# Kernel tuning notes

Measured on AMD Instinct MI355X. Metric: run time of the kernel, lower is better.

The kernel has to match this reference:

```python
import jax, jax.numpy as jnp
import numpy as np

D_EEG_MAX = 10.0
H_FMRI_MAX = 5.0
CLZ_MAX = 3.0
D_MAX = 1.0  # config.diffusion_coefficient_range[1]
N_LEVELS = 8  # discretization levels -> 64 pair-histogram bins


def setup_inputs() -> dict:
    key = jax.random.key(0)
    k1, k2 = jax.random.split(key)
    B, E = 8192, 4096
    psi_distribution = jax.random.uniform(k1, (B, E), dtype=jnp.float32)
    fractal_field = jax.random.normal(k2, (B, E), dtype=jnp.float32)
    fci_weights = jnp.array([0.4, 0.3, 0.3], dtype=jnp.float32)
    return {"psi_distribution": psi_distribution,
            "fractal_field": fractal_field,
            "fci_weights": fci_weights}


def _d_eeg(psi):
    # entropy of P(psi) per row, averaged; torch.std is unbiased (ddof=1)
    entropy = -jnp.sum(psi * jnp.log(psi + 1e-10), axis=-1).mean()
    spatial_variation = jnp.std(psi, axis=-1, ddof=1).mean()
    return jnp.minimum(entropy * spatial_variation * 3.0, D_EEG_MAX)


def _spatial_correlation(field):
    # Pearson corr between adjacent feature columns over the batch, vectorized
    c = field - field.mean(axis=0, keepdims=True)          # [B, E]
    var = jnp.sum(c * c, axis=0)                            # [E]
    cov = jnp.sum(c[:, :-1] * c[:, 1:], axis=0)             # [E-1]
    corr = cov / jnp.sqrt(var[:-1] * var[1:])               # [E-1]
    mask = ~jnp.isnan(corr)                                 # torch code skips NaNs
    n = jnp.sum(mask)
    mean_corr = jnp.where(n > 0,
                          jnp.sum(jnp.where(mask, corr, 0.0)) / jnp.maximum(n, 1),
                          0.0)
    return jnp.abs(mean_corr)


def _h_fmri(field):
    field_magnitude = jnp.linalg.norm(field, axis=-1).mean()
    correlation = _spatial_correlation(field)
    return jnp.minimum(field_magnitude * correlation * 2.0, H_FMRI_MAX)


def _conditional_entropy(psi):
    # discretize to 8 levels; count (curr,next) pairs with a 64-bin histogram
    q = jnp.clip(jnp.floor(psi * N_LEVELS), 0, N_LEVELS - 1).astype(jnp.int32)  # [B, E]
    pair_ids = (q[:, :-1] * N_LEVELS + q[:, 1:]).reshape(-1)                    # [B*(E-1)]
    counts = jnp.zeros((N_LEVELS * N_LEVELS,), jnp.float32).at[pair_ids].add(1.0)
    total = pair_ids.shape[0]  # static
    p = counts / total
    return -jnp.sum(jnp.where(p > 0, p * jnp.log2(jnp.where(p > 0, p, 1.0)), 0.0))


def _clz(psi, field):
    cond_ent = _conditional_entropy(psi)
    field_complexity = jnp.std(field, ddof=1)  # torch.std over all elems, unbiased
    return jnp.minimum(cond_ent + 0.3 * field_complexity, CLZ_MAX)


def reference(psi_distribution, fractal_field, fci_weights):
    d_eeg = _d_eeg(psi_distribution)
    h_fmri = _h_fmri(fractal_field)
    clz = _clz(psi_distribution, fractal_field)
    fci_num = (fci_weights[0] * (d_eeg / D_EEG_MAX)
               + fci_weights[1] * (h_fmri / H_FMRI_MAX)
               + fci_weights[2] * (clz / CLZ_MAX))
    return jnp.clip(fci_num / D_MAX, 0.0, 1.0)
```

## Files before the change

kernel.cpp:

```cpp
#include <hip/hip_runtime.h>
#include <math.h>

#define BATCH 8192
#define EDIM  4096
#define NBINS 64
#define NREP  64


__global__ __launch_bounds__(256) void psi_pass(const float* __restrict__ psi,
                                                unsigned* __restrict__ ghist,
                                                float* __restrict__ row_ent,
                                                float* __restrict__ row_std) {
  const int r = blockIdx.x;
  const int t = threadIdx.x;
  const float4* row = (const float4*)(psi + (size_t)r * EDIM);

  __shared__ unsigned lhist[NBINS];
  __shared__ float firsts[EDIM / 4];
  __shared__ float red[12];

  if (t < NBINS) lhist[t] = 0u;

  float4 v[4];
#pragma unroll
  for (int k = 0; k < 4; ++k) v[k] = row[t + k * 256];
#pragma unroll
  for (int k = 0; k < 4; ++k) firsts[t + k * 256] = v[k].x;
  __syncthreads();

  float s = 0.f, sq = 0.f, pl = 0.f;
#pragma unroll
  for (int k = 0; k < 4; ++k) {
    const int vi = t + k * 256;
    float ee[4] = {v[k].x, v[k].y, v[k].z, v[k].w};
    int q[4];
#pragma unroll
    for (int j = 0; j < 4; ++j) {
      float x = ee[j];
      s += x;
      sq += x * x;
      pl += x * __logf(x + 1e-10f);
      int qq = (int)floorf(x * 8.0f);
      q[j] = min(max(qq, 0), 7);
    }
#pragma unroll
    for (int j = 0; j < 3; ++j)
      atomicAdd(&lhist[q[j] * 8 + q[j + 1]], 1u);
    if (vi < EDIM / 4 - 1) {
      float xn = firsts[vi + 1];
      int qn = min(max((int)floorf(xn * 8.0f), 0), 7);
      atomicAdd(&lhist[q[3] * 8 + qn], 1u);
    }
  }

  for (int off = 32; off; off >>= 1) {
    s  += __shfl_down(s, off);
    sq += __shfl_down(sq, off);
    pl += __shfl_down(pl, off);
  }
  const int w = t >> 6, lane = t & 63;
  if (lane == 0) { red[w] = s; red[4 + w] = sq; red[8 + w] = pl; }
  __syncthreads();
  if (t == 0) {
    float S  = red[0] + red[1] + red[2] + red[3];
    float SQ = red[4] + red[5] + red[6] + red[7];
    float PL = red[8] + red[9] + red[10] + red[11];
    row_ent[r] = -PL;
    float var = (SQ - S * S / (float)EDIM) / (float)(EDIM - 1);
    row_std[r] = sqrtf(fmaxf(var, 0.f));
  }
  if (t < NBINS) atomicAdd(&ghist[(blockIdx.x & (NREP - 1)) * NBINS + t], lhist[t]);
}

__global__ __launch_bounds__(256) void field_pass(const float* __restrict__ f,
                                                  float* __restrict__ colsum,
                                                  float* __restrict__ colsumsq,
                                                  float* __restrict__ pairprod,
                                                  float* __restrict__ row_fsq) {
  const int gw = (blockIdx.x * 256 + threadIdx.x) >> 6;
  const int lane = threadIdx.x & 63;
  const int cchunk = gw & 15;
  const int rgroup = gw >> 4;
  const int c0 = cchunk * 256 + lane * 4;
  const int r0 = rgroup * (BATCH / 512);
  const bool lastCol = (c0 + 3 == EDIM - 1);

  float cs0 = 0.f, cs1 = 0.f, cs2 = 0.f, cs3 = 0.f;
  float cq0 = 0.f, cq1 = 0.f, cq2 = 0.f, cq3 = 0.f;
  float pp0 = 0.f, pp1 = 0.f, pp2 = 0.f, pp3 = 0.f;
#pragma unroll 4
  for (int i = 0; i < BATCH / 512; ++i) {
    const int r = r0 + i;
    const float* rowp = f + (size_t)r * EDIM;
    const float4 v = *(const float4*)(rowp + c0);
    cs0 += v.x; cs1 += v.y; cs2 += v.z; cs3 += v.w;
    cq0 += v.x * v.x; cq1 += v.y * v.y; cq2 += v.z * v.z; cq3 += v.w * v.w;
    pp0 += v.x * v.y; pp1 += v.y * v.z; pp2 += v.z * v.w;
    float nx = __shfl_down(v.x, 1);
    if (lane == 63 && !lastCol) nx = rowp[c0 + 4];
    if (!lastCol) pp3 += v.w * nx;
    float rs = v.x * v.x + v.y * v.y + v.z * v.z + v.w * v.w;
    for (int off = 32; off; off >>= 1) rs += __shfl_down(rs, off);
    if (lane == 0) atomicAdd(&row_fsq[r], rs);
  }
  atomicAdd(&colsum[c0 + 0], cs0);  atomicAdd(&colsumsq[c0 + 0], cq0);
  atomicAdd(&colsum[c0 + 1], cs1);  atomicAdd(&colsumsq[c0 + 1], cq1);
  atomicAdd(&colsum[c0 + 2], cs2);  atomicAdd(&colsumsq[c0 + 2], cq2);
  atomicAdd(&colsum[c0 + 3], cs3);  atomicAdd(&colsumsq[c0 + 3], cq3);
  atomicAdd(&pairprod[c0 + 0], pp0);
  atomicAdd(&pairprod[c0 + 1], pp1);
  atomicAdd(&pairprod[c0 + 2], pp2);
  if (!lastCol) atomicAdd(&pairprod[c0 + 3], pp3);
}

__device__ double blk_reduce(double v, double* sbuf) {
  const int t = threadIdx.x;
  for (int off = 32; off; off >>= 1) v += __shfl_down(v, off);
  __syncthreads();
  if ((t & 63) == 0) sbuf[t >> 6] = v;
  __syncthreads();
  return sbuf[0] + sbuf[1] + sbuf[2] + sbuf[3];
}

__global__ __launch_bounds__(256) void finalize(const unsigned* __restrict__ ghist,
                                                const float* __restrict__ row_ent,
                                                const float* __restrict__ row_std,
                                                const float* __restrict__ row_fsq,
                                                const float* __restrict__ colsum,
                                                const float* __restrict__ colsumsq,
                                                const float* __restrict__ pairprod,
                                                const float* __restrict__ wts,
                                                float* __restrict__ out) {
  const int t = threadIdx.x;
  __shared__ double sbuf[4];

  double se = 0, ss = 0, sm = 0;
  for (int i = t; i < BATCH; i += 256) {
    se += (double)row_ent[i];
    ss += (double)row_std[i];
    sm += (double)sqrtf(row_fsq[i]);
  }
  double SE = blk_reduce(se, sbuf);
  double SS = blk_reduce(ss, sbuf);
  double SM = blk_reduce(sm, sbuf);

  double csum = 0, ccnt = 0;
  for (int e = t; e < EDIM - 1; e += 256) {
    double sa = colsum[e], sb = colsum[e + 1];
    double va = (double)colsumsq[e]     - sa * sa / (double)BATCH;
    double vb = (double)colsumsq[e + 1] - sb * sb / (double)BATCH;
    double cov = (double)pairprod[e] - sa * sb / (double)BATCH;
    double corr = cov / sqrt(va * vb);
    if (!isnan(corr)) { csum += corr; ccnt += 1.0; }
  }
  double CS = blk_reduce(csum, sbuf);
  double CN = blk_reduce(ccnt, sbuf);

  double gs = 0, gq = 0;
  for (int e = t; e < EDIM; e += 256) { gs += (double)colsum[e]; gq += (double)colsumsq[e]; }
  double GS = blk_reduce(gs, sbuf);
  double GQ = blk_reduce(gq, sbuf);

  double hent = 0;
  if (t < NBINS) {
    unsigned long long cnt = 0;
    for (int rrep = 0; rrep < NREP; ++rrep) cnt += (unsigned long long)ghist[rrep * NBINS + t];
    const double total = (double)BATCH * (double)(EDIM - 1);
    double p = (double)cnt / total;
    if (p > 0.0) hent = -p * log2(p);
  }
  double HE = blk_reduce(hent, sbuf);

  if (t == 0) {
    double entropy = SE / (double)BATCH;
    double spat = SS / (double)BATCH;
    double d_eeg = fmin(entropy * spat * 3.0, 10.0);

    double mag = SM / (double)BATCH;
    double mean_corr = (CN > 0.0) ? (CS / CN) : 0.0;
    double h_fmri = fmin(mag * fabs(mean_corr) * 2.0, 5.0);

    double Nf = (double)BATCH * (double)EDIM;
    double gvar = (GQ - GS * GS / Nf) / (Nf - 1.0);
    double fstd = sqrt(fmax(gvar, 0.0));
    double clz = fmin(HE + 0.3 * fstd, 3.0);

    double fci = (double)wts[0] * (d_eeg / 10.0)
               + (double)wts[1] * (h_fmri / 5.0)
               + (double)wts[2] * (clz / 3.0);
    fci = fmin(fmax(fci, 0.0), 1.0);
    out[0] = (float)fci;
  }
}

extern "C" void kernel_launch(void* const* d_in, const int* in_sizes, int n_in,
                              void* d_out, int out_size, void* d_ws, size_t ws_size,
                              hipStream_t stream) {
  const float* psi = (const float*)d_in[0];
  const float* fld = (const float*)d_in[1];
  const float* wts = (const float*)d_in[2];
  float* out = (float*)d_out;

  char* ws = (char*)d_ws;
  unsigned* ghist = (unsigned*)(ws);
  float* row_ent  = (float*)(ws + 16384);
  float* row_std  = (float*)(ws + 49152);
  float* row_fsq  = (float*)(ws + 81920);
  float* colsum   = (float*)(ws + 114688);
  float* colsumsq = (float*)(ws + 131072);
  float* pairprod = (float*)(ws + 147456);

  hipMemsetAsync(d_ws, 0, 163840, stream);

  psi_pass<<<BATCH, 256, 0, stream>>>(psi, ghist, row_ent, row_std);
  field_pass<<<2048, 256, 0, stream>>>(fld, colsum, colsumsq, pairprod, row_fsq);
  finalize<<<1, 256, 0, stream>>>(ghist, row_ent, row_std, row_fsq,
                                  colsum, colsumsq, pairprod, wts, out);
}
```

Measured before the change: 416.4 us.

## Replace global atomics with partial-sum buffers and a dedicated reduce kernel

When the workspace is large enough, per-block histograms and per-row-group column partial sums are written straight to scratch buffers instead of being accumulated with global atomics. A new reduce kernel sums the partials and computes the chunk-boundary pair products by re-reading the field, which also removes the per-iteration scalar load in the inner loop. The memset is dropped on this path. It costs extra scratch traffic (several MB of partials) and one more kernel launch. The old atomic path is kept as a fallback for small workspaces.

```diff
diff --git a/kernel.cpp b/kernel.cpp
--- a/kernel.cpp
+++ b/kernel.cpp
@@ -4,13 +4,31 @@
 #define BATCH 8192
 #define EDIM  4096
 #define NBINS 64
-#define NREP  64
+#define NGRP  128
+#define ROWSW (BATCH / NGRP)
+#define NCHK  16
+#define NREP_FB 64
+
+#define OFF_HISTP   0u
+#define OFF_CSP     (2u * 1024 * 1024 / 4)
+#define OFF_CQP     (4u * 1024 * 1024 / 4)
+#define OFF_PPP     (6u * 1024 * 1024 / 4)
+#define OFF_RFSQP   (8u * 1024 * 1024 / 4)
+#define OFF_ROWENT  (OFF_RFSQP + NCHK * BATCH)
+#define OFF_ROWSTD  (OFF_ROWENT + BATCH)
+#define OFF_ROWFSQ  (OFF_ROWSTD + BATCH)
+#define OFF_COLSUM  (OFF_ROWFSQ + BATCH)
+#define OFF_COLSQ   (OFF_COLSUM + EDIM)
+#define OFF_PAIRP   (OFF_COLSQ + EDIM)
+#define OFF_HIST2   (OFF_PAIRP + EDIM)
+#define PRIMARY_WS_BYTES ((OFF_HIST2 + 2 * NBINS) * 4)
 
 
 __global__ __launch_bounds__(256) void psi_pass(const float* __restrict__ psi,
-                                                unsigned* __restrict__ ghist,
+                                                unsigned* __restrict__ hist,
                                                 float* __restrict__ row_ent,
-                                                float* __restrict__ row_std) {
+                                                float* __restrict__ row_std,
+                                                int fb) {
   const int r = blockIdx.x;
   const int t = threadIdx.x;
   const float4* row = (const float4*)(psi + (size_t)r * EDIM);
@@ -69,37 +87,73 @@
     float var = (SQ - S * S / (float)EDIM) / (float)(EDIM - 1);
     row_std[r] = sqrtf(fmaxf(var, 0.f));
   }
-  if (t < NBINS) atomicAdd(&ghist[(blockIdx.x & (NREP - 1)) * NBINS + t], lhist[t]);
+  if (t < NBINS) {
+    if (fb) atomicAdd(&hist[(size_t)(r & (NREP_FB - 1)) * NBINS + t], lhist[t]);
+    else    hist[(size_t)r * NBINS + t] = lhist[t];
+  }
 }
 
 __global__ __launch_bounds__(256) void field_pass(const float* __restrict__ f,
-                                                  float* __restrict__ colsum,
-                                                  float* __restrict__ colsumsq,
-                                                  float* __restrict__ pairprod,
-                                                  float* __restrict__ row_fsq) {
+                                                  float* __restrict__ cs_part,
+                                                  float* __restrict__ cq_part,
+                                                  float* __restrict__ pp_part,
+                                                  float* __restrict__ rfsq_part) {
+  const int gw = (blockIdx.x * 256 + threadIdx.x) >> 6;
+  const int lane = threadIdx.x & 63;
+  const int cchunk = gw & (NCHK - 1);
+  const int g = gw >> 4;
+  const int c0 = cchunk * 256 + lane * 4;
+  const int r0 = g * ROWSW;
+
+  float cs0 = 0.f, cs1 = 0.f, cs2 = 0.f, cs3 = 0.f;
+  float cq0 = 0.f, cq1 = 0.f, cq2 = 0.f, cq3 = 0.f;
+  float pp0 = 0.f, pp1 = 0.f, pp2 = 0.f, pp3 = 0.f;
+#pragma unroll 8
+  for (int i = 0; i < ROWSW; ++i) {
+    const int r = r0 + i;
+    const float4 v = *(const float4*)(f + (size_t)r * EDIM + c0);
+    cs0 += v.x; cs1 += v.y; cs2 += v.z; cs3 += v.w;
+    cq0 = fmaf(v.x, v.x, cq0); cq1 = fmaf(v.y, v.y, cq1);
+    cq2 = fmaf(v.z, v.z, cq2); cq3 = fmaf(v.w, v.w, cq3);
+    pp0 = fmaf(v.x, v.y, pp0); pp1 = fmaf(v.y, v.z, pp1); pp2 = fmaf(v.z, v.w, pp2);
+    float nx = __shfl_down(v.x, 1);
+    if (lane != 63) pp3 = fmaf(v.w, nx, pp3);
+    float rs = fmaf(v.x, v.x, fmaf(v.y, v.y, fmaf(v.z, v.z, v.w * v.w)));
+    for (int off = 32; off; off >>= 1) rs += __shfl_down(rs, off);
+    if (lane == 0) rfsq_part[(size_t)cchunk * BATCH + r] = rs;
+  }
+  const size_t cb = (size_t)g * EDIM + c0;
+  *(float4*)(cs_part + cb) = make_float4(cs0, cs1, cs2, cs3);
+  *(float4*)(cq_part + cb) = make_float4(cq0, cq1, cq2, cq3);
+  *(float4*)(pp_part + cb) = make_float4(pp0, pp1, pp2, pp3);
+}
+
+__global__ __launch_bounds__(256) void field_pass_fb(const float* __restrict__ f,
+                                                     float* __restrict__ colsum,
+                                                     float* __restrict__ colsumsq,
+                                                     float* __restrict__ pairprod,
+                                                     float* __restrict__ row_fsq) {
   const int gw = (blockIdx.x * 256 + threadIdx.x) >> 6;
   const int lane = threadIdx.x & 63;
   const int cchunk = gw & 15;
   const int rgroup = gw >> 4;
   const int c0 = cchunk * 256 + lane * 4;
   const int r0 = rgroup * (BATCH / 512);
-  const bool lastCol = (c0 + 3 == EDIM - 1);
 
   float cs0 = 0.f, cs1 = 0.f, cs2 = 0.f, cs3 = 0.f;
   float cq0 = 0.f, cq1 = 0.f, cq2 = 0.f, cq3 = 0.f;
   float pp0 = 0.f, pp1 = 0.f, pp2 = 0.f, pp3 = 0.f;
-#pragma unroll 4
+#pragma unroll 8
   for (int i = 0; i < BATCH / 512; ++i) {
     const int r = r0 + i;
-    const float* rowp = f + (size_t)r * EDIM;
-    const float4 v = *(const float4*)(rowp + c0);
+    const float4 v = *(const float4*)(f + (size_t)r * EDIM + c0);
     cs0 += v.x; cs1 += v.y; cs2 += v.z; cs3 += v.w;
-    cq0 += v.x * v.x; cq1 += v.y * v.y; cq2 += v.z * v.z; cq3 += v.w * v.w;
-    pp0 += v.x * v.y; pp1 += v.y * v.z; pp2 += v.z * v.w;
+    cq0 = fmaf(v.x, v.x, cq0); cq1 = fmaf(v.y, v.y, cq1);
+    cq2 = fmaf(v.z, v.z, cq2); cq3 = fmaf(v.w, v.w, cq3);
+    pp0 = fmaf(v.x, v.y, pp0); pp1 = fmaf(v.y, v.z, pp1); pp2 = fmaf(v.z, v.w, pp2);
     float nx = __shfl_down(v.x, 1);
-    if (lane == 63 && !lastCol) nx = rowp[c0 + 4];
-    if (!lastCol) pp3 += v.w * nx;
-    float rs = v.x * v.x + v.y * v.y + v.z * v.z + v.w * v.w;
+    if (lane != 63) pp3 = fmaf(v.w, nx, pp3);
+    float rs = fmaf(v.x, v.x, fmaf(v.y, v.y, fmaf(v.z, v.z, v.w * v.w)));
     for (int off = 32; off; off >>= 1) rs += __shfl_down(rs, off);
     if (lane == 0) atomicAdd(&row_fsq[r], rs);
   }
@@ -110,7 +164,75 @@
   atomicAdd(&pairprod[c0 + 0], pp0);
   atomicAdd(&pairprod[c0 + 1], pp1);
   atomicAdd(&pairprod[c0 + 2], pp2);
-  if (!lastCol) atomicAdd(&pairprod[c0 + 3], pp3);
+  if (lane != 63) atomicAdd(&pairprod[c0 + 3], pp3);
+}
+
+__global__ __launch_bounds__(256) void boundary_pass(const float* __restrict__ f,
+                                                     float* __restrict__ pairprod) {
+  __shared__ float sred[4];
+  const int c = blockIdx.x * 256 + 255;
+  const int t = threadIdx.x;
+  float acc = 0.f;
+  for (int r = t; r < BATCH; r += 256)
+    acc = fmaf(f[(size_t)r * EDIM + c], f[(size_t)r * EDIM + c + 1], acc);
+  for (int off = 32; off; off >>= 1) acc += __shfl_down(acc, off);
+  if ((t & 63) == 0) sred[t >> 6] = acc;
+  __syncthreads();
+  if (t == 0) pairprod[c] = sred[0] + sred[1] + sred[2] + sred[3];
+}
+
+__global__ __launch_bounds__(256) void reduce_pass(const float* __restrict__ f,
+                                                   const unsigned* __restrict__ hist_part,
+                                                   const float* __restrict__ cs_part,
+                                                   const float* __restrict__ cq_part,
+                                                   const float* __restrict__ pp_part,
+                                                   const float* __restrict__ rfsq_part,
+                                                   float* __restrict__ colsum,
+                                                   float* __restrict__ colsumsq,
+                                                   float* __restrict__ pairprod,
+                                                   float* __restrict__ row_fsq,
+                                                   unsigned* __restrict__ hist2) {
+  const int b = blockIdx.x;
+  const int t = threadIdx.x;
+
+  if (b < 48) {
+    const int stat = b >> 4;
+    const int c = (b & 15) * 256 + t;
+    const float* part = (stat == 0) ? cs_part : (stat == 1) ? cq_part : pp_part;
+    float acc = 0.f;
+#pragma unroll 8
+    for (int g = 0; g < NGRP; ++g) acc += part[(size_t)g * EDIM + c];
+    if (stat == 0) colsum[c] = acc;
+    else if (stat == 1) colsumsq[c] = acc;
+    else if ((c & 255) != 255) pairprod[c] = acc;
+  } else if (b < 80) {
+    const int r = (b - 48) * 256 + t;
+    float acc = 0.f;
+#pragma unroll
+    for (int k = 0; k < NCHK; ++k) acc += rfsq_part[(size_t)k * BATCH + r];
+    row_fsq[r] = acc;
+  } else if (b < 88) {
+    __shared__ unsigned hred[4][NBINS];
+    const int j = b - 80;
+    const int bin = t & 63, quad = t >> 6;
+    unsigned acc = 0u;
+    for (int pb = j * 1024 + quad; pb < (j + 1) * 1024; pb += 4)
+      acc += hist_part[(size_t)pb * NBINS + bin];
+    hred[quad][bin] = acc;
+    __syncthreads();
+    if (t < NBINS)
+      hist2[(size_t)j * NBINS + t] = hred[0][t] + hred[1][t] + hred[2][t] + hred[3][t];
+  } else {
+    __shared__ float sred[4];
+    const int c = (b - 88) * 256 + 255;
+    float acc = 0.f;
+    for (int r = t; r < BATCH; r += 256)
+      acc = fmaf(f[(size_t)r * EDIM + c], f[(size_t)r * EDIM + c + 1], acc);
+    for (int off = 32; off; off >>= 1) acc += __shfl_down(acc, off);
+    if ((t & 63) == 0) sred[t >> 6] = acc;
+    __syncthreads();
+    if (t == 0) pairprod[c] = sred[0] + sred[1] + sred[2] + sred[3];
+  }
 }
 
 __device__ double blk_reduce(double v, double* sbuf) {
@@ -122,7 +244,8 @@
   return sbuf[0] + sbuf[1] + sbuf[2] + sbuf[3];
 }
 
-__global__ __launch_bounds__(256) void finalize(const unsigned* __restrict__ ghist,
+__global__ __launch_bounds__(256) void finalize(const unsigned* __restrict__ hist,
+                                                int nreps,
                                                 const float* __restrict__ row_ent,
                                                 const float* __restrict__ row_std,
                                                 const float* __restrict__ row_fsq,
@@ -164,7 +287,7 @@
   double hent = 0;
   if (t < NBINS) {
     unsigned long long cnt = 0;
-    for (int rrep = 0; rrep < NREP; ++rrep) cnt += (unsigned long long)ghist[rrep * NBINS + t];
+    for (int j = 0; j < nreps; ++j) cnt += (unsigned long long)hist[(size_t)j * NBINS + t];
     const double total = (double)BATCH * (double)(EDIM - 1);
     double p = (double)cnt / total;
     if (p > 0.0) hent = -p * log2(p);
@@ -200,20 +323,43 @@
   const float* fld = (const float*)d_in[1];
   const float* wts = (const float*)d_in[2];
   float* out = (float*)d_out;
-
-  char* ws = (char*)d_ws;
-  unsigned* ghist = (unsigned*)(ws);
-  float* row_ent  = (float*)(ws + 16384);
-  float* row_std  = (float*)(ws + 49152);
-  float* row_fsq  = (float*)(ws + 81920);
-  float* colsum   = (float*)(ws + 114688);
-  float* colsumsq = (float*)(ws + 131072);
-  float* pairprod = (float*)(ws + 147456);
-
-  hipMemsetAsync(d_ws, 0, 163840, stream);
-
-  psi_pass<<<BATCH, 256, 0, stream>>>(psi, ghist, row_ent, row_std);
-  field_pass<<<2048, 256, 0, stream>>>(fld, colsum, colsumsq, pairprod, row_fsq);
-  finalize<<<1, 256, 0, stream>>>(ghist, row_ent, row_std, row_fsq,
-                                  colsum, colsumsq, pairprod, wts, out);
-}
+  float* ws = (float*)d_ws;
+
+  if (ws_size >= (size_t)PRIMARY_WS_BYTES) {
+    unsigned* hist_part = (unsigned*)(ws + OFF_HISTP);
+    float* cs_part   = ws + OFF_CSP;
+    float* cq_part   = ws + OFF_CQP;
+    float* pp_part   = ws + OFF_PPP;
+    float* rfsq_part = ws + OFF_RFSQP;
+    float* row_ent   = ws + OFF_ROWENT;
+    float* row_std   = ws + OFF_ROWSTD;
+    float* row_fsq   = ws + OFF_ROWFSQ;
+    float* colsum    = ws + OFF_COLSUM;
+    float* colsumsq  = ws + OFF_COLSQ;
+    float* pairprod  = ws + OFF_PAIRP;
+    unsigned* hist2  = (unsigned*)(ws + OFF_HIST2);
+
+    psi_pass<<<BATCH, 256, 0, stream>>>(psi, hist_part, row_ent, row_std, 0);
+    field_pass<<<(NGRP * NCHK) / 4, 256, 0, stream>>>(fld, cs_part, cq_part, pp_part, rfsq_part);
+    reduce_pass<<<103, 256, 0, stream>>>(fld, hist_part, cs_part, cq_part, pp_part,
+                                         rfsq_part, colsum, colsumsq, pairprod, row_fsq, hist2);
+    finalize<<<1, 256, 0, stream>>>(hist2, 8, row_ent, row_std, row_fsq,
+                                    colsum, colsumsq, pairprod, wts, out);
+  } else {
+    char* wb = (char*)d_ws;
+    unsigned* ghist = (unsigned*)(wb);
+    float* row_ent  = (float*)(wb + 16384);
+    float* row_std  = (float*)(wb + 49152);
+    float* row_fsq  = (float*)(wb + 81920);
+    float* colsum   = (float*)(wb + 114688);
+    float* colsumsq = (float*)(wb + 131072);
+    float* pairprod = (float*)(wb + 147456);
+
+    hipMemsetAsync(d_ws, 0, 163840, stream);
+    psi_pass<<<BATCH, 256, 0, stream>>>(psi, ghist, row_ent, row_std, 1);
+    field_pass_fb<<<2048, 256, 0, stream>>>(fld, colsum, colsumsq, pairprod, row_fsq);
+    boundary_pass<<<15, 256, 0, stream>>>(fld, pairprod);
+    finalize<<<1, 256, 0, stream>>>(ghist, NREP_FB, row_ent, row_std, row_fsq,
+                                    colsum, colsumsq, pairprod, wts, out);
+  }
+}
```

New measurement: 351.8 us. 1.18x faster.
